# Kernel tuning notes

Measured on AMD Instinct MI355X. Metric: run time of the kernel, lower is better.

Reference implementation:

```python
import jax, jax.numpy as jnp
import numpy as np

TOPK = 2  # config.expert_topk


def setup_inputs() -> dict:
    key = jax.random.key(0)
    k1, k2, k3, k4 = jax.random.split(key, 4)
    B, T, D, H, E = 2, 2048, 768, 3072, 8
    x = jax.random.normal(k1, (B, T, D), jnp.float32)
    gate_w = jax.random.normal(k2, (E, D), jnp.float32) * 0.02   # nn.Linear(D, E).weight
    w_fc = jax.random.normal(k3, (E, H, D), jnp.float32) * 0.02  # per-expert c_fc.weight [out,in]
    w_proj = jax.random.normal(k4, (E, D, H), jnp.float32) * 0.02  # per-expert c_proj.weight
    return {"x": x, "gate_w": gate_w, "w_fc": w_fc, "w_proj": w_proj}


def reference(x, gate_w, w_fc, w_proj):
    # x: [B,T,D]; gate_w: [E,D]; w_fc: [E,H,D]; w_proj: [E,D,H]
    B, T, D = x.shape
    E = gate_w.shape[0]
    N = B * T
    xf = x.reshape(N, D)

    gate_logits = xf @ gate_w.T                       # [N,E]
    gate_probs = jax.nn.softmax(gate_logits, axis=-1)
    rw, idx = jax.lax.top_k(gate_probs, TOPK)          # [N,k]
    rw = rw / jnp.sum(rw, axis=-1, keepdims=True)

    # combine[n,e] = sum_k rw[n,k] * (idx[n,k]==e); zero for unselected experts,
    # so the dense per-expert MLP below computes the same math as torch dispatch.
    oh = jax.nn.one_hot(idx, E, dtype=xf.dtype)        # [N,k,E]
    combine = jnp.einsum('nk,nke->ne', rw, oh)         # [N,E]

    h = jnp.einsum('nd,ehd->neh', xf, w_fc)            # [N,E,H]
    h = jnp.square(jax.nn.relu(h))                     # relu(x)^2
    y = jnp.einsum('neh,edh->ned', h, w_proj)          # [N,E,D]
    out = jnp.einsum('ned,ne->nd', y, combine).reshape(B, T, D)

    # expert_freq = bincount(expert_indices)/N, detached in the loss
    counts = jnp.sum(oh, axis=(0, 1))                  # [E]
    expert_freq = counts / N
    balance_loss = jnp.sum(gate_probs.mean(axis=0) * jax.lax.stop_gradient(expert_freq)) * E
    return out, balance_loss
```

## Files before the change

kernel.cpp:

```cpp
#include <hip/hip_runtime.h>
#include <hip/hip_bf16.h>

typedef __bf16 bf16_t;
typedef bf16_t bf16x8 __attribute__((ext_vector_type(8)));
typedef bf16_t bf16x4 __attribute__((ext_vector_type(4)));
typedef float f32x4 __attribute__((ext_vector_type(4)));

#define N_TOK 4096
#define DIM   768
#define HID   3072
#define NEXP  8
#define PADROWS 9216
#define MMAX  32
#define MT2   64

#define OFF_COUNTS 0
#define OFF_PSUM   32
#define OFF_OFFPAD 64
#define OFF_CURSOR 128
#define OFF_TOKE   256
#define OFF_TOKW   (OFF_TOKE + 4*8192)
#define OFF_PERMT  (OFF_TOKW + 4*8192)
#define OFF_PERMW  (OFF_PERMT + 4*PADROWS)
#define OFF_XP     (((OFF_PERMW + 4*PADROWS) + 511) & ~511ull)
#define OFF_WFC    (OFF_XP + 2ull*PADROWS*DIM)
#define OFF_WPJ    (OFF_WFC + 2ull*NEXP*HID*DIM)
#define OFF_H      (OFF_WPJ + 2ull*NEXP*DIM*HID)
#define WS_NEEDED  (OFF_H + 2ull*PADROWS*HID)

#define GATE_BLOCKS (N_TOK / 4)
#define CONVH_BLOCKS 4608
#define GEMM1_BLOCKS (8 * 24 * MMAX)

__device__ __forceinline__ void async_copy16(const bf16_t* g, bf16_t* l) {
    __builtin_amdgcn_global_load_lds(
        (const __attribute__((address_space(1))) void*)g,
        (__attribute__((address_space(3))) void*)l, 16, 0, 0);
}

__device__ __forceinline__ void convert_chunk(const float* __restrict__ src,
                                              bf16_t* __restrict__ dst,
                                              int cid, int t) {
    const long long base = (long long)cid * 256 + t;
    const long long stride = (long long)CONVH_BLOCKS * 256;
#pragma unroll
    for (int it = 0; it < 4; it++) {
        const long long i4 = base + (long long)it * stride;
        float4 v = *((const float4*)src + i4);
        bf16x4 o;
        o[0] = (bf16_t)v.x; o[1] = (bf16_t)v.y;
        o[2] = (bf16_t)v.z; o[3] = (bf16_t)v.w;
        *(bf16x4*)(dst + i4 * 4) = o;
    }
}

__global__ __launch_bounds__(256) void prep_kernel(
    const float* __restrict__ w_fc, bf16_t* __restrict__ wfc_b,
    const float* __restrict__ x, const float* __restrict__ gw,
    int* __restrict__ cs_part, float* __restrict__ ps_part,
    int* __restrict__ tok_e, float* __restrict__ tok_w)
{
    __shared__ float ps[8];
    __shared__ int cs[8];

    if (blockIdx.x >= GATE_BLOCKS) {
        convert_chunk(w_fc, wfc_b, blockIdx.x - GATE_BLOCKS, threadIdx.x);
        return;
    }

    if (threadIdx.x < 8) { ps[threadIdx.x] = 0.f; cs[threadIdx.x] = 0; }
    __syncthreads();

    const int bid = blockIdx.x;
    const int wv = threadIdx.x >> 6, lane = threadIdx.x & 63;
    const int n = bid * 4 + wv;

    float acc[8];
#pragma unroll
    for (int e = 0; e < 8; e++) acc[e] = 0.f;
    const float* xr = x + (size_t)n * DIM;
#pragma unroll
    for (int c = 0; c < 12; c++) {
        const float xv = xr[c * 64 + lane];
#pragma unroll
        for (int e = 0; e < 8; e++) acc[e] += xv * gw[e * DIM + c * 64 + lane];
    }
#pragma unroll
    for (int e = 0; e < 8; e++)
        for (int off = 32; off > 0; off >>= 1) acc[e] += __shfl_xor(acc[e], off, 64);

    float mx = acc[0];
#pragma unroll
    for (int e = 1; e < 8; e++) mx = fmaxf(mx, acc[e]);
    float p[8], s = 0.f;
#pragma unroll
    for (int e = 0; e < 8; e++) { p[e] = expf(acc[e] - mx); s += p[e]; }

    int e1 = 0;
#pragma unroll
    for (int e = 1; e < 8; e++) if (p[e] > p[e1]) e1 = e;
    int e2 = (e1 == 0) ? 1 : 0;
#pragma unroll
    for (int e = 0; e < 8; e++) if (e != e1 && p[e] > p[e2]) e2 = e;
    const float denom = p[e1] + p[e2];

    if (lane == 0) {
        tok_e[2 * n] = e1; tok_e[2 * n + 1] = e2;
        tok_w[2 * n] = p[e1] / denom; tok_w[2 * n + 1] = p[e2] / denom;
        const float inv = 1.f / s;
#pragma unroll
        for (int e = 0; e < 8; e++) atomicAdd(&ps[e], p[e] * inv);
        atomicAdd(&cs[e1], 1); atomicAdd(&cs[e2], 1);
    }
    __syncthreads();
    if (threadIdx.x < 8) {
        ps_part[bid * 8 + threadIdx.x] = ps[threadIdx.x];
        cs_part[bid * 8 + threadIdx.x] = cs[threadIdx.x];
    }
}

__global__ __launch_bounds__(256) void finalize_scatter(
    const int* cs_part, const float* ps_part,
    const int* __restrict__ tok_e, const float* __restrict__ tok_w,
    int* __restrict__ counts, int* __restrict__ off_pad,
    int* perm_tok, int* inv_pos, float* __restrict__ out_loss)
{
    __shared__ float rps[256];
    __shared__ int rcs[256];
    __shared__ int s_cur[8];
    const int t = threadIdx.x;
    const int e = t & 7, chunk = t >> 3;
    float psum = 0.f; int csum = 0;
#pragma unroll
    for (int i = 0; i < 32; i++) {
        const int b = chunk * 32 + i;
        psum += ps_part[b * 8 + e];
        csum += cs_part[b * 8 + e];
    }
    rps[t] = psum; rcs[t] = csum;
    __syncthreads();
    for (int s = 128; s >= 8; s >>= 1) {
        if (t < s) { rps[t] += rps[t + s]; rcs[t] += rcs[t + s]; }
        __syncthreads();
    }
    if (t == 0) {
        int off = 0; float loss = 0.f;
        for (int k = 0; k < 8; k++) {
            counts[k] = rcs[k];
            off_pad[k] = off; s_cur[k] = off;
            off += ((rcs[k] + 127) & ~127);
            loss += rps[k] * (float)rcs[k];
        }
        off_pad[8] = off;
        *out_loss = loss * 8.f / ((float)N_TOK * (float)N_TOK);
    }
    __syncthreads();
    for (int r = 0; r < N_TOK / 256; r++) {
        const int n = r * 256 + t;
#pragma unroll
        for (int k = 0; k < 2; k++) {
            const int ee = tok_e[2 * n + k];
            const int pos = atomicAdd(&s_cur[ee], 1);
            perm_tok[pos] = n;
            inv_pos[2 * n + k] = pos;
        }
    }
}

__global__ __launch_bounds__(256) void gather_x_kernel(
    const float* __restrict__ x, const int* __restrict__ off_pad,
    const int* __restrict__ counts, const int* __restrict__ perm_tok,
    bf16_t* __restrict__ xp)
{
    __shared__ int so[9], scnt[8];
    if (threadIdx.x < 9) so[threadIdx.x] = off_pad[threadIdx.x];
    if (threadIdx.x < 8) scnt[threadIdx.x] = counts[threadIdx.x];
    __syncthreads();
    const int gid = blockIdx.x * 256 + threadIdx.x;
    const int p = gid / 192;
    const int c = (gid - p * 192) * 4;
    int e = 0;
#pragma unroll
    for (int k = 1; k < 8; k++) if (p >= so[k]) e = k;
    const bool valid = (p < so[8]) && (p - so[e] < scnt[e]);
    float4 v = make_float4(0.f, 0.f, 0.f, 0.f);
    if (valid) {
        const int tok = perm_tok[p];
        v = *(const float4*)(x + (size_t)tok * DIM + c);
    }
    bf16x4 o; o[0] = (bf16_t)v.x; o[1] = (bf16_t)v.y; o[2] = (bf16_t)v.z; o[3] = (bf16_t)v.w;
    *(bf16x4*)(xp + (size_t)p * DIM + c) = o;
}

__global__ __launch_bounds__(256, 4) void gemm1_kernel(
    const bf16_t* __restrict__ xp, const bf16_t* __restrict__ wfc,
    const int* __restrict__ off_pad, bf16_t* __restrict__ h,
    const float* __restrict__ w_proj, bf16_t* __restrict__ wpj_b)
{
    const int id = blockIdx.x;
    if (id >= GEMM1_BLOCKS) {
        convert_chunk(w_proj, wpj_b, id - GEMM1_BLOCKS, threadIdx.x);
        return;
    }
    const int e = id & 7;
    const int slot = id >> 3;
    const int n_t = slot / MMAX, m_t = slot % MMAX;

    const int seg0 = off_pad[e];
    const int cnt_pad = off_pad[e + 1] - seg0;
    const int m0 = m_t * 128;
    if (m0 >= cnt_pad) return;
    const int n0 = n_t * 128;

    __shared__ bf16_t As[128 * 64];
    __shared__ bf16_t Bs[128 * 64];

    const int t = threadIdx.x;
    const int srow = t >> 3, sc = t & 7;
    const int gsc = sc ^ (srow & 7);
    const bf16_t* abase = xp + (size_t)(seg0 + m0 + srow) * DIM + gsc * 8;
    const bf16_t* bbase = wfc + ((size_t)e * HID + n0 + srow) * DIM + gsc * 8;

    const int wv = t >> 6, lane = t & 63;
    const int lrow = lane & 15, quad = lane >> 4;
    const int wm = (wv & 1) * 64, wn = (wv >> 1) * 64;
    const int sw = lrow & 7;

    f32x4 acc[4][4] = {};

    for (int k0 = 0; k0 < DIM; k0 += 64) {
        __syncthreads();
#pragma unroll
        for (int ii = 0; ii < 4; ii++) {
            async_copy16(abase + (size_t)ii * 32 * DIM + k0, &As[(ii * 256 + t) * 8]);
            async_copy16(bbase + (size_t)ii * 32 * DIM + k0, &Bs[(ii * 256 + t) * 8]);
        }
        __syncthreads();
#pragma unroll
        for (int kh = 0; kh < 2; kh++) {
            const int ch = ((kh * 4 + quad) ^ sw) * 8;
            bf16x8 af[4], bfv[4];
#pragma unroll
            for (int i = 0; i < 4; i++)
                af[i] = *(bf16x8*)&As[(wm + i * 16 + lrow) * 64 + ch];
#pragma unroll
            for (int j = 0; j < 4; j++)
                bfv[j] = *(bf16x8*)&Bs[(wn + j * 16 + lrow) * 64 + ch];
#pragma unroll
            for (int i = 0; i < 4; i++)
#pragma unroll
                for (int j = 0; j < 4; j++)
                    acc[i][j] = __builtin_amdgcn_mfma_f32_16x16x32_bf16(af[i], bfv[j], acc[i][j], 0, 0, 0);
        }
    }

#pragma unroll
    for (int i = 0; i < 4; i++) {
#pragma unroll
        for (int g = 0; g < 4; g++) {
            const int m = m0 + wm + i * 16 + quad * 4 + g;
            bf16_t* hrow = h + (size_t)(seg0 + m) * HID + n0 + wn + lrow;
#pragma unroll
            for (int j = 0; j < 4; j++) {
                float v = fmaxf(acc[i][j][g], 0.f);
                hrow[j * 16] = (bf16_t)(v * v);
            }
        }
    }
}

__global__ __launch_bounds__(256, 3) void gemm2_kernel(
    const bf16_t* __restrict__ h, const bf16_t* __restrict__ wpj,
    const int* __restrict__ off_pad, const int* __restrict__ counts,
    bf16_t* __restrict__ y)
{
    const int id = blockIdx.x;
    const int e = id & 7;
    const int slot = id >> 3;
    const int m_t = slot / 6, n_t = slot % 6;

    const int seg0 = off_pad[e];
    const int cnt = counts[e];
    const int m0 = m_t * 64;
    if (m0 >= cnt) return;
    const int n0 = n_t * 128;

    __shared__ bf16_t As[2][64 * 64];
    __shared__ bf16_t Bs[2][128 * 64];

    const int t = threadIdx.x;
    const int srow = t >> 3, sc = t & 7;
    const int gsc = sc ^ (srow & 7);
    const bf16_t* abase = h + (size_t)(seg0 + m0 + srow) * HID + gsc * 8;
    const bf16_t* bbase = wpj + ((size_t)e * DIM + n0 + srow) * HID + gsc * 8;

    const int wv = t >> 6, lane = t & 63;
    const int lrow = lane & 15, quad = lane >> 4;
    const int wm = (wv & 1) * 32, wn = (wv >> 1) * 64;
    const int sw = lrow & 7;

    f32x4 acc[2][4] = {};

    for (int k0 = 0; k0 < HID; k0 += 128) {
        __syncthreads();
#pragma unroll
        for (int p = 0; p < 2; p++) {
#pragma unroll
            for (int ii = 0; ii < 2; ii++)
                async_copy16(abase + (size_t)ii * 32 * HID + k0 + p * 64,
                             &As[p][(ii * 256 + t) * 8]);
#pragma unroll
            for (int ii = 0; ii < 4; ii++)
                async_copy16(bbase + (size_t)ii * 32 * HID + k0 + p * 64,
                             &Bs[p][(ii * 256 + t) * 8]);
        }
        __syncthreads();
#pragma unroll
        for (int kh = 0; kh < 4; kh++) {
            const int p = kh >> 1, khh = kh & 1;
            const int ch = ((khh * 4 + quad) ^ sw) * 8;
            bf16x8 af[2], bfv[4];
#pragma unroll
            for (int i = 0; i < 2; i++)
                af[i] = *(bf16x8*)&As[p][(wm + i * 16 + lrow) * 64 + ch];
#pragma unroll
            for (int j = 0; j < 4; j++)
                bfv[j] = *(bf16x8*)&Bs[p][(wn + j * 16 + lrow) * 64 + ch];
#pragma unroll
            for (int i = 0; i < 2; i++)
#pragma unroll
                for (int j = 0; j < 4; j++)
                    acc[i][j] = __builtin_amdgcn_mfma_f32_16x16x32_bf16(af[i], bfv[j], acc[i][j], 0, 0, 0);
        }
    }

#pragma unroll
    for (int i = 0; i < 2; i++) {
#pragma unroll
        for (int g = 0; g < 4; g++) {
            const int m = m0 + wm + i * 16 + quad * 4 + g;
            if (m < cnt) {
                bf16_t* yrow = y + (size_t)(seg0 + m) * DIM + n0 + wn + lrow;
#pragma unroll
                for (int j = 0; j < 4; j++)
                    yrow[j * 16] = (bf16_t)acc[i][j][g];
            }
        }
    }
}

__global__ __launch_bounds__(192) void combine_kernel(
    const bf16_t* __restrict__ y, const int* __restrict__ inv_pos,
    const float* __restrict__ tok_w, float* __restrict__ out)
{
    const int n = blockIdx.x;
    const int d = threadIdx.x * 4;
    const int p1 = inv_pos[2 * n], p2 = inv_pos[2 * n + 1];
    const float w1 = tok_w[2 * n], w2 = tok_w[2 * n + 1];
    bf16x4 a = *(const bf16x4*)(y + (size_t)p1 * DIM + d);
    bf16x4 b = *(const bf16x4*)(y + (size_t)p2 * DIM + d);
    float4 o;
    o.x = w1 * (float)a[0] + w2 * (float)b[0];
    o.y = w1 * (float)a[1] + w2 * (float)b[1];
    o.z = w1 * (float)a[2] + w2 * (float)b[2];
    o.w = w1 * (float)a[3] + w2 * (float)b[3];
    *(float4*)(out + (size_t)n * DIM + d) = o;
}

extern "C" void kernel_launch(void* const* d_in, const int* in_sizes, int n_in,
                              void* d_out, int out_size, void* d_ws, size_t ws_size,
                              hipStream_t stream) {
    const float* x      = (const float*)d_in[0];
    const float* gate_w = (const float*)d_in[1];
    const float* w_fc   = (const float*)d_in[2];
    const float* w_proj = (const float*)d_in[3];
    float* out = (float*)d_out;

    if (ws_size < WS_NEEDED) return;

    char* w = (char*)d_ws;
    int*    counts    = (int*)(w + OFF_COUNTS);
    int*    off_pad   = (int*)(w + OFF_OFFPAD);
    int*    tok_e     = (int*)(w + OFF_TOKE);
    float*  tok_w     = (float*)(w + OFF_TOKW);
    int*    perm_tok  = (int*)(w + OFF_PERMT);
    int*    inv_pos   = (int*)(w + OFF_PERMW);
    bf16_t* xp        = (bf16_t*)(w + OFF_XP);
    bf16_t* wfc_b     = (bf16_t*)(w + OFF_WFC);
    bf16_t* wpj_b     = (bf16_t*)(w + OFF_WPJ);
    bf16_t* hbuf      = (bf16_t*)(w + OFF_H);

    int*   cs_part = perm_tok;
    float* ps_part = (float*)inv_pos;
    bf16_t* y = xp;

    prep_kernel<<<GATE_BLOCKS + CONVH_BLOCKS, 256, 0, stream>>>(
        w_fc, wfc_b, x, gate_w, cs_part, ps_part, tok_e, tok_w);
    finalize_scatter<<<1, 256, 0, stream>>>(cs_part, ps_part, tok_e, tok_w,
                                            counts, off_pad, perm_tok, inv_pos,
                                            out + (size_t)out_size - 1);
    gather_x_kernel<<<PADROWS * DIM / 4 / 256, 256, 0, stream>>>(x, off_pad, counts, perm_tok, xp);

    gemm1_kernel<<<GEMM1_BLOCKS + CONVH_BLOCKS, 256, 0, stream>>>(
        xp, wfc_b, off_pad, hbuf, w_proj, wpj_b);
    gemm2_kernel<<<8 * MT2 * 6, 256, 0, stream>>>(hbuf, wpj_b, off_pad, counts, y);
    combine_kernel<<<N_TOK, 192, 0, stream>>>(y, inv_pos, tok_w, out);
}
```

Baseline: 317.7 us.

## Split-K gemm2 into two halves with 128x128 tiles, sum partials in combine

The second expert GEMM now uses 128x128 output tiles (up from 64x128) with a single-stage 64-wide K step, and splits the 3072-long reduction into two halves written to separate bf16 partial buffers. The combine kernel reads both partials and adds them before applying the routing weights. This aims to raise per-block data reuse while keeping enough blocks in flight for occupancy. The cost is extra partial-buffer traffic, an added bf16 rounding of each partial, and reuse of the w_fc bf16 buffer as scratch. The weight-conversion loads also become nontemporal.

```diff
diff --git a/kernel.cpp b/kernel.cpp
--- a/kernel.cpp
+++ b/kernel.cpp
@@ -12,7 +12,6 @@
 #define NEXP  8
 #define PADROWS 9216
 #define MMAX  32
-#define MT2   64
 
 #define OFF_COUNTS 0
 #define OFF_PSUM   32
@@ -46,7 +45,7 @@
 #pragma unroll
     for (int it = 0; it < 4; it++) {
         const long long i4 = base + (long long)it * stride;
-        float4 v = *((const float4*)src + i4);
+        f32x4 v = __builtin_nontemporal_load(((const f32x4*)src) + i4);
         bf16x4 o;
         o[0] = (bf16_t)v.x; o[1] = (bf16_t)v.y;
         o[2] = (bf16_t)v.z; o[3] = (bf16_t)v.w;
@@ -269,78 +268,75 @@
     }
 }
 
-__global__ __launch_bounds__(256, 3) void gemm2_kernel(
+__global__ __launch_bounds__(256, 4) void gemm2_kernel(
     const bf16_t* __restrict__ h, const bf16_t* __restrict__ wpj,
     const int* __restrict__ off_pad, const int* __restrict__ counts,
-    bf16_t* __restrict__ y)
+    bf16_t* __restrict__ y0, bf16_t* __restrict__ y1)
 {
     const int id = blockIdx.x;
     const int e = id & 7;
     const int slot = id >> 3;
-    const int m_t = slot / 6, n_t = slot % 6;
+    const int split = slot / (MMAX * 6);
+    const int rem = slot % (MMAX * 6);
+    const int m_t = rem / 6, n_t = rem % 6;
 
     const int seg0 = off_pad[e];
     const int cnt = counts[e];
-    const int m0 = m_t * 64;
+    const int m0 = m_t * 128;
     if (m0 >= cnt) return;
     const int n0 = n_t * 128;
-
-    __shared__ bf16_t As[2][64 * 64];
-    __shared__ bf16_t Bs[2][128 * 64];
+    const int kbeg = split * (HID / 2);
+
+    __shared__ bf16_t As[128 * 64];
+    __shared__ bf16_t Bs[128 * 64];
 
     const int t = threadIdx.x;
     const int srow = t >> 3, sc = t & 7;
     const int gsc = sc ^ (srow & 7);
-    const bf16_t* abase = h + (size_t)(seg0 + m0 + srow) * HID + gsc * 8;
-    const bf16_t* bbase = wpj + ((size_t)e * DIM + n0 + srow) * HID + gsc * 8;
+    const bf16_t* abase = h + (size_t)(seg0 + m0 + srow) * HID + kbeg + gsc * 8;
+    const bf16_t* bbase = wpj + ((size_t)e * DIM + n0 + srow) * HID + kbeg + gsc * 8;
 
     const int wv = t >> 6, lane = t & 63;
     const int lrow = lane & 15, quad = lane >> 4;
-    const int wm = (wv & 1) * 32, wn = (wv >> 1) * 64;
+    const int wm = (wv & 1) * 64, wn = (wv >> 1) * 64;
     const int sw = lrow & 7;
 
-    f32x4 acc[2][4] = {};
-
-    for (int k0 = 0; k0 < HID; k0 += 128) {
+    f32x4 acc[4][4] = {};
+
+    for (int k0 = 0; k0 < HID / 2; k0 += 64) {
         __syncthreads();
 #pragma unroll
-        for (int p = 0; p < 2; p++) {
-#pragma unroll
-            for (int ii = 0; ii < 2; ii++)
-                async_copy16(abase + (size_t)ii * 32 * HID + k0 + p * 64,
-                             &As[p][(ii * 256 + t) * 8]);
-#pragma unroll
-            for (int ii = 0; ii < 4; ii++)
-                async_copy16(bbase + (size_t)ii * 32 * HID + k0 + p * 64,
-                             &Bs[p][(ii * 256 + t) * 8]);
+        for (int ii = 0; ii < 4; ii++) {
+            async_copy16(abase + (size_t)ii * 32 * HID + k0, &As[(ii * 256 + t) * 8]);
+            async_copy16(bbase + (size_t)ii * 32 * HID + k0, &Bs[(ii * 256 + t) * 8]);
         }
         __syncthreads();
 #pragma unroll
-        for (int kh = 0; kh < 4; kh++) {
-            const int p = kh >> 1, khh = kh & 1;
-            const int ch = ((khh * 4 + quad) ^ sw) * 8;
-            bf16x8 af[2], bfv[4];
-#pragma unroll
-            for (int i = 0; i < 2; i++)
-                af[i] = *(bf16x8*)&As[p][(wm + i * 16 + lrow) * 64 + ch];
+        for (int kh = 0; kh < 2; kh++) {
+            const int ch = ((kh * 4 + quad) ^ sw) * 8;
+            bf16x8 af[4], bfv[4];
+#pragma unroll
+            for (int i = 0; i < 4; i++)
+                af[i] = *(bf16x8*)&As[(wm + i * 16 + lrow) * 64 + ch];
 #pragma unroll
             for (int j = 0; j < 4; j++)
-                bfv[j] = *(bf16x8*)&Bs[p][(wn + j * 16 + lrow) * 64 + ch];
-#pragma unroll
-            for (int i = 0; i < 2; i++)
+                bfv[j] = *(bf16x8*)&Bs[(wn + j * 16 + lrow) * 64 + ch];
+#pragma unroll
+            for (int i = 0; i < 4; i++)
 #pragma unroll
                 for (int j = 0; j < 4; j++)
                     acc[i][j] = __builtin_amdgcn_mfma_f32_16x16x32_bf16(af[i], bfv[j], acc[i][j], 0, 0, 0);
         }
     }
 
-#pragma unroll
-    for (int i = 0; i < 2; i++) {
+    bf16_t* yout = split ? y1 : y0;
+#pragma unroll
+    for (int i = 0; i < 4; i++) {
 #pragma unroll
         for (int g = 0; g < 4; g++) {
             const int m = m0 + wm + i * 16 + quad * 4 + g;
             if (m < cnt) {
-                bf16_t* yrow = y + (size_t)(seg0 + m) * DIM + n0 + wn + lrow;
+                bf16_t* yrow = yout + (size_t)(seg0 + m) * DIM + n0 + wn + lrow;
 #pragma unroll
                 for (int j = 0; j < 4; j++)
                     yrow[j * 16] = (bf16_t)acc[i][j][g];
@@ -350,20 +346,23 @@
 }
 
 __global__ __launch_bounds__(192) void combine_kernel(
-    const bf16_t* __restrict__ y, const int* __restrict__ inv_pos,
-    const float* __restrict__ tok_w, float* __restrict__ out)
+    const bf16_t* __restrict__ y0, const bf16_t* __restrict__ y1,
+    const int* __restrict__ inv_pos, const float* __restrict__ tok_w,
+    float* __restrict__ out)
 {
     const int n = blockIdx.x;
     const int d = threadIdx.x * 4;
     const int p1 = inv_pos[2 * n], p2 = inv_pos[2 * n + 1];
     const float w1 = tok_w[2 * n], w2 = tok_w[2 * n + 1];
-    bf16x4 a = *(const bf16x4*)(y + (size_t)p1 * DIM + d);
-    bf16x4 b = *(const bf16x4*)(y + (size_t)p2 * DIM + d);
+    bf16x4 a0 = *(const bf16x4*)(y0 + (size_t)p1 * DIM + d);
+    bf16x4 a1 = *(const bf16x4*)(y1 + (size_t)p1 * DIM + d);
+    bf16x4 b0 = *(const bf16x4*)(y0 + (size_t)p2 * DIM + d);
+    bf16x4 b1 = *(const bf16x4*)(y1 + (size_t)p2 * DIM + d);
     float4 o;
-    o.x = w1 * (float)a[0] + w2 * (float)b[0];
-    o.y = w1 * (float)a[1] + w2 * (float)b[1];
-    o.z = w1 * (float)a[2] + w2 * (float)b[2];
-    o.w = w1 * (float)a[3] + w2 * (float)b[3];
+    o.x = w1 * ((float)a0[0] + (float)a1[0]) + w2 * ((float)b0[0] + (float)b1[0]);
+    o.y = w1 * ((float)a0[1] + (float)a1[1]) + w2 * ((float)b0[1] + (float)b1[1]);
+    o.z = w1 * ((float)a0[2] + (float)a1[2]) + w2 * ((float)b0[2] + (float)b1[2]);
+    o.w = w1 * ((float)a0[3] + (float)a1[3]) + w2 * ((float)b0[3] + (float)b1[3]);
     *(float4*)(out + (size_t)n * DIM + d) = o;
 }
 
@@ -392,7 +391,8 @@
 
     int*   cs_part = perm_tok;
     float* ps_part = (float*)inv_pos;
-    bf16_t* y = xp;
+    bf16_t* y0 = xp;
+    bf16_t* y1 = wfc_b;
 
     prep_kernel<<<GATE_BLOCKS + CONVH_BLOCKS, 256, 0, stream>>>(
         w_fc, wfc_b, x, gate_w, cs_part, ps_part, tok_e, tok_w);
@@ -403,6 +403,6 @@
 
     gemm1_kernel<<<GEMM1_BLOCKS + CONVH_BLOCKS, 256, 0, stream>>>(
         xp, wfc_b, off_pad, hbuf, w_proj, wpj_b);
-    gemm2_kernel<<<8 * MT2 * 6, 256, 0, stream>>>(hbuf, wpj_b, off_pad, counts, y);
-    combine_kernel<<<N_TOK, 192, 0, stream>>>(y, inv_pos, tok_w, out);
-}
+    gemm2_kernel<<<8 * 2 * MMAX * 6, 256, 0, stream>>>(hbuf, wpj_b, off_pad, counts, y0, y1);
+    combine_kernel<<<N_TOK, 192, 0, stream>>>(y0, y1, inv_pos, tok_w, out);
+}
```

New measurement: 297.9 us. 1.07x faster.
